# Kernel tuning notes

Measured on AMD Instinct MI355X. Metric: run time of the kernel, lower is better.

The kernel has to match this reference:

```python
import jax, jax.numpy as jnp
import numpy as np

L, H = 4, 8
BIAS_STEP = 25
LN_EPS = 1e-5

def make_pe(T, D):
    pos = np.arange(T)[:, None].astype(np.float32)
    div = np.exp(np.arange(0, D, 2).astype(np.float32) * (-np.log(10000.0) / D))
    pe = np.zeros((T, D), np.float32)
    pe[:, 0::2] = np.sin(pos * div)
    pe[:, 1::2] = np.cos(pos * div)
    return jnp.asarray(pe)

def make_band_mask(T):
    # (H, T, T) bool, True = masked out. Head h attends within |i-j| <= BIAS_STEP*(h+1).
    i = np.arange(T)
    dist = np.abs(i[:, None] - i[None, :])
    win = (np.arange(H) + 1) * BIAS_STEP
    return jnp.asarray(dist[None, :, :] > win[:, None, None])

def layer_norm(x, g, b):
    m = x.mean(-1, keepdims=True)
    v = ((x - m) ** 2).mean(-1, keepdims=True)
    return (x - m) * jax.lax.rsqrt(v + LN_EPS) * g + b

def setup_inputs() -> dict:
    key = jax.random.key(0)
    ks = jax.random.split(key, 16)
    s = 0.02
    BS, T, IN, D, FF, C = 8, 1000, 256, 512, 2048, 8
    return {
        'x': jax.random.normal(ks[0], (BS, T, IN), jnp.float32),
        'Wemb': jax.random.normal(ks[1], (D, IN), jnp.float32) * s,
        'bemb': jnp.zeros((D,), jnp.float32),
        'Wqkv': jax.random.normal(ks[2], (L, 3 * D, D), jnp.float32) * s,
        'bqkv': jnp.zeros((L, 3 * D), jnp.float32),
        'Wo': jax.random.normal(ks[3], (L, D, D), jnp.float32) * s,
        'bo': jnp.zeros((L, D), jnp.float32),
        'W1': jax.random.normal(ks[4], (L, FF, D), jnp.float32) * s,
        'b1f': jnp.zeros((L, FF), jnp.float32),
        'W2': jax.random.normal(ks[5], (L, D, FF), jnp.float32) * s,
        'b2f': jnp.zeros((L, D), jnp.float32),
        'g1': jnp.ones((L, D), jnp.float32),
        'be1': jnp.zeros((L, D), jnp.float32),
        'g2': jnp.ones((L, D), jnp.float32),
        'be2': jnp.zeros((L, D), jnp.float32),
        'Wcls': jax.random.normal(ks[6], (C, D), jnp.float32) * s,
        'bcls': jnp.zeros((C,), jnp.float32),
    }

def reference(x, Wemb, bemb, Wqkv, bqkv, Wo, bo, W1, b1f, W2, b2f, g1, be1, g2, be2, Wcls, bcls):
    bs, T, _ = x.shape
    D = Wemb.shape[0]
    dh = D // H
    h = x @ Wemb.T + bemb                     # (bs,T,D) input embedding
    h = h + make_pe(T, D)[None]               # sinusoidal PE (dropout=0)
    mask = make_band_mask(T)                  # (H,T,T)
    neg = jnp.finfo(h.dtype).min
    for l in range(L):                        # post-norm TransformerEncoderLayer
        qkv = h @ Wqkv[l].T + bqkv[l]
        q, k, v = jnp.split(qkv, 3, axis=-1)
        q = q.reshape(bs, T, H, dh).transpose(0, 2, 1, 3)
        k = k.reshape(bs, T, H, dh).transpose(0, 2, 1, 3)
        v = v.reshape(bs, T, H, dh).transpose(0, 2, 1, 3)
        s = jnp.einsum('bhqd,bhkd->bhqk', q, k) / jnp.sqrt(jnp.asarray(dh, h.dtype))
        s = jnp.where(mask[None], neg, s)
        a = jax.nn.softmax(s, axis=-1)
        o = jnp.einsum('bhqk,bhkd->bhqd', a, v).transpose(0, 2, 1, 3).reshape(bs, T, D)
        o = o @ Wo[l].T + bo[l]
        h = layer_norm(h + o, g1[l], be1[l])
        ff = jax.nn.relu(h @ W1[l].T + b1f[l]) @ W2[l].T + b2f[l]
        h = layer_norm(h + ff, g2[l], be2[l])
    pooled = h.max(axis=1)                    # global max pool over time (max_pool=True)
    logits = pooled @ Wcls.T + bcls
    return jax.nn.log_softmax(logits, axis=1)
```

## Files before the change

### kernel.cpp

```cpp
#include <hip/hip_runtime.h>
#include <math.h>

#define T_SEQ   1000
#define BATCH   8
#define DMODEL  512
#define NHEAD   8
#define DHEAD   64
#define FFDIM   2048
#define NLAYER  4
#define MROWS   (BATCH * T_SEQ)
#define TCHUNK  25
#define QKS     1024
#define VTS     1024

typedef __bf16 bf16x8 __attribute__((ext_vector_type(8)));
typedef __bf16 bf16x4 __attribute__((ext_vector_type(4)));
typedef float  f32x4  __attribute__((ext_vector_type(4)));
typedef float  f32x16 __attribute__((ext_vector_type(16)));

#define GL2LDS(g, l) \
    __builtin_amdgcn_global_load_lds((const __attribute__((address_space(1))) void*)(g), \
                                     (__attribute__((address_space(3))) void*)(l), 16, 0, 0)

struct F2BFArgs {
    const float* src[6];
    __bf16*      dst[6];
    int          off[7];
};

__global__ __launch_bounds__(256)
void f2bf_all(F2BFArgs a)
{
    const int blk = blockIdx.x;
    int seg = 0;
    #pragma unroll
    for (int s = 1; s < 6; ++s)
        if (blk >= a.off[s]) seg = s;
    const int i = (blk - a.off[seg]) * 1024 + threadIdx.x * 4;
    float4 v = *(const float4*)(a.src[seg] + i);
    bf16x4 o;
    o[0] = (__bf16)v.x; o[1] = (__bf16)v.y; o[2] = (__bf16)v.z; o[3] = (__bf16)v.w;
    *(bf16x4*)(a.dst[seg] + i) = o;
}

template<int MODE, bool RELU>
__global__ __launch_bounds__(256)
void gemm_bf16(const __bf16* __restrict__ A, const __bf16* __restrict__ B,
               const float* __restrict__ bias, __bf16* __restrict__ Cb,
               __bf16* __restrict__ Vt, int M, int N, int K)
{
    __shared__ __align__(16) __bf16 As[3][64 * 64];
    __shared__ __align__(16) __bf16 Bs[3][128 * 64];

    const int tid  = threadIdx.x;
    const int lane = tid & 63;
    const int w    = tid >> 6;
    const int wr   = w >> 1, wc = w & 1;

    const int gx  = gridDim.x;
    const int nwg = gx * gridDim.y;
    const int bid = blockIdx.y * gx + blockIdx.x;
    const int qc  = nwg >> 3, rc = nwg & 7;
    const int xcd = bid & 7, idx = bid >> 3;
    const int swz = (xcd < rc) ? xcd * (qc + 1) + idx
                               : rc * (qc + 1) + (xcd - rc) * qc + idx;
    const int row0 = (swz / gx) * 64;
    const int col0 = (swz % gx) * 128;

    size_t aoffg[2], boffg[4];
    int    ldso[4];
    #pragma unroll
    for (int p = 0; p < 4; ++p) {
        const int bo = p * 4096 + tid * 16;
        const int r  = bo >> 7;
        const int cs = (bo & 127) ^ ((r & 7) << 4);
        if (p < 2) aoffg[p] = (size_t)(row0 + r) * K * 2 + cs;
        boffg[p] = (size_t)(col0 + r) * K * 2 + cs;
        ldso[p]  = bo;
    }

    f32x4 acc[2][4];
    #pragma unroll
    for (int m = 0; m < 2; ++m)
        #pragma unroll
        for (int n = 0; n < 4; ++n) acc[m][n] = (f32x4)0.f;

    const char* gA = (const char*)A;
    const char* gB = (const char*)B;
    const int nt = K >> 6;

    auto STAGE = [&](int tt, int buf) {
        const size_t kb = (size_t)tt << 7;
        char* lA = (char*)As[buf];
        char* lB = (char*)Bs[buf];
        #pragma unroll
        for (int p = 0; p < 2; ++p) GL2LDS(gA + aoffg[p] + kb, lA + ldso[p]);
        #pragma unroll
        for (int p = 0; p < 4; ++p) GL2LDS(gB + boffg[p] + kb, lB + ldso[p]);
    };

    STAGE(0, 0);
    STAGE(1, 1);
    asm volatile("s_waitcnt vmcnt(6)" ::: "memory");
    __builtin_amdgcn_s_barrier();
    __builtin_amdgcn_sched_barrier(0);

    int bc = 0, bn = 2;
    for (int t = 0; t < nt; ++t) {
        if (t + 2 < nt) STAGE(t + 2, bn);
        const char* as = (const char*)As[bc];
        const char* bs = (const char*)Bs[bc];
        __builtin_amdgcn_s_setprio(1);
        #pragma unroll
        for (int ks = 0; ks < 2; ++ks) {
            bf16x8 af[2], bfr[4];
            const int cb = ks * 64 + (lane >> 4) * 16;
            #pragma unroll
            for (int m = 0; m < 2; ++m) {
                const int rr = wr * 32 + m * 16 + (lane & 15);
                af[m] = *(const bf16x8*)(as + rr * 128 + (cb ^ ((rr & 7) << 4)));
            }
            #pragma unroll
            for (int n = 0; n < 4; ++n) {
                const int rr = wc * 64 + n * 16 + (lane & 15);
                bfr[n] = *(const bf16x8*)(bs + rr * 128 + (cb ^ ((rr & 7) << 4)));
            }
            #pragma unroll
            for (int m = 0; m < 2; ++m)
                #pragma unroll
                for (int n = 0; n < 4; ++n)
                    acc[m][n] = __builtin_amdgcn_mfma_f32_16x16x32_bf16(af[m], bfr[n], acc[m][n], 0, 0, 0);
        }
        __builtin_amdgcn_s_setprio(0);
        if (t + 2 < nt) { asm volatile("s_waitcnt vmcnt(6)" ::: "memory"); }
        else            { asm volatile("s_waitcnt vmcnt(0)" ::: "memory"); }
        __builtin_amdgcn_s_barrier();
        __builtin_amdgcn_sched_barrier(0);
        bc = bc + 1; if (bc == 3) bc = 0;
        bn = bn + 1; if (bn == 3) bn = 0;
    }

    const int crow = (lane >> 4) * 4;
    const int ccol = lane & 15;

    if (MODE == 2 && col0 >= 1024) {
        __bf16* vtl = &Bs[0][0];
        #pragma unroll
        for (int n = 0; n < 4; ++n) {
            const int dl = wc * 64 + n * 16 + ccol;
            const float bv = bias[col0 + dl];
            #pragma unroll
            for (int m = 0; m < 2; ++m) {
                const int tl0 = wr * 32 + m * 16 + crow;
                #pragma unroll
                for (int r = 0; r < 4; ++r)
                    vtl[dl * 68 + tl0 + r] = (__bf16)(acc[m][n][r] + bv);
            }
        }
        __syncthreads();
        const int dbase = col0 - 1024;
        #pragma unroll
        for (int pass = 0; pass < 4; ++pass) {
            const int dl = pass * 32 + (tid >> 3);
            const int tc = (tid & 7) * 8;
            const int gr = row0 + tc;
            const bf16x8 vv = *(const bf16x8*)(vtl + dl * 68 + tc);
            const int bidx = gr / T_SEQ;
            const int tt   = gr - bidx * T_SEQ;
            __bf16* dst = Vt + (((size_t)(bidx * DMODEL + dbase + dl)) << 10) + tt;
            if (tt + 8 <= T_SEQ) {
                *(bf16x8*)dst = vv;
            } else {
                #pragma unroll
                for (int e = 0; e < 8; ++e) {
                    const int gre = gr + e;
                    const int be = gre / T_SEQ, te = gre - be * T_SEQ;
                    Vt[(((size_t)(be * DMODEL + dbase + dl)) << 10) + te] = vv[e];
                }
            }
        }
        return;
    }

    #pragma unroll
    for (int n = 0; n < 4; ++n) {
        const int gc = col0 + wc * 64 + n * 16 + ccol;
        const float bv = bias[gc];
        float freq = 0.f;
        if (MODE == 1) freq = __expf((float)(gc & ~1) * (-9.210340371976184f / (float)DMODEL));
        #pragma unroll
        for (int m = 0; m < 2; ++m) {
            const int gr0 = row0 + wr * 32 + m * 16 + crow;
            #pragma unroll
            for (int r = 0; r < 4; ++r) {
                const int gr = gr0 + r;
                float v = acc[m][n][r] + bv;
                if (MODE == 1) {
                    const int tt = gr % T_SEQ;
                    const float ang = (float)tt * freq;
                    v += (gc & 1) ? __cosf(ang) : __sinf(ang);
                }
                if (RELU) v = fmaxf(v, 0.f);
                if (MODE == 2) {
                    Cb[(size_t)gr * QKS + gc] = (__bf16)v;
                } else {
                    Cb[(size_t)gr * N + gc] = (__bf16)v;
                }
            }
        }
    }
}

__global__ __launch_bounds__(64)
void attn_mfma(const __bf16* __restrict__ qkb, const __bf16* __restrict__ vt,
               __bf16* __restrict__ o)
{
    const int wv   = blockIdx.x;
    const int lane = threadIdx.x;
    const int hh   = wv & 7;
    const int qt   = (wv >> 3) & 31;
    const int b    = wv >> 8;
    const int qb   = qt * 32;
    const int half = lane >> 5;
    const int ql   = lane & 31;
    const int i    = qb + ql;
    const int iq   = (i < T_SEQ) ? i : (T_SEQ - 1);
    const float C2 = 0.125f * 1.44269504089f;

    const __bf16* Q = qkb + (size_t)b * T_SEQ * QKS + hh * DHEAD;
    const __bf16* K = Q + 512;
    const __bf16* Vb = vt + (((size_t)b * DMODEL + hh * DHEAD) << 10);

    bf16x8 qf[4];
    {
        const __bf16* qrow = Q + (size_t)iq * QKS + half * 8;
        #pragma unroll
        for (int ds = 0; ds < 4; ++ds)
            qf[ds] = *(const bf16x8*)(qrow + ds * 16);
    }

    const int w = 25 * (hh + 1);
    const int kb_lo = (qb - w > 0 ? qb - w : 0) & ~31;
    const int kb_hi = (qb + 31 + w < T_SEQ - 1) ? (qb + 31 + w) : (T_SEQ - 1);
    const int spanv = (2 * w < T_SEQ - 1 - i + w) ? 2 * w : (T_SEQ - 1 - i + w);
    const unsigned span = (unsigned)spanv;

    float m2 = -1e9f, l = 0.f;
    f32x16 oa0 = (f32x16)0.f, oa1 = (f32x16)0.f;

    for (int kb = kb_lo; kb <= kb_hi; kb += 32) {
        f32x16 sv = (f32x16)0.f;
        {
            int krow = kb + ql; if (krow > T_SEQ - 1) krow = T_SEQ - 1;
            const __bf16* kr = K + (size_t)krow * QKS + half * 8;
            #pragma unroll
            for (int ds = 0; ds < 4; ++ds) {
                bf16x8 kf = *(const bf16x8*)(kr + ds * 16);
                sv = __builtin_amdgcn_mfma_f32_32x32x16_bf16(kf, qf[ds], sv, 0, 0, 0);
            }
        }

        const bool full = (kb >= qb + 31 - w) && (kb + 31 <= qb + w)
                       && (kb + 31 <= T_SEQ - 1);
        float s2[16];
        if (full) {
            #pragma unroll
            for (int r = 0; r < 16; ++r) s2[r] = sv[r] * C2;
        } else {
            const int base = kb - i + w;
            #pragma unroll
            for (int r = 0; r < 16; ++r) {
                const int kr = (r & 3) + 8 * (r >> 2) + 4 * half;
                const unsigned jrel = (unsigned)(base + kr);
                s2[r] = (jrel <= span) ? sv[r] * C2 : -1e9f;
            }
        }

        float mx = s2[0];
        #pragma unroll
        for (int r = 1; r < 16; ++r) mx = fmaxf(mx, s2[r]);
        mx = fmaxf(mx, __shfl_xor(mx, 32, 64));

        if (!__all(mx <= m2 + 8.0f)) {
            const float mnew  = fmaxf(m2, mx);
            const float scale = exp2f(m2 - mnew);
            m2 = mnew;
            l *= scale;
            oa0 *= scale;
            oa1 *= scale;
        }

        float p[16];
        float ps = 0.f;
        #pragma unroll
        for (int r = 0; r < 16; ++r) { p[r] = exp2f(s2[r] - m2); ps += p[r]; }
        ps += __shfl_xor(ps, 32, 64);
        l += ps;

        unsigned pk[8];
        #pragma unroll
        for (int t = 0; t < 8; ++t) {
            union { unsigned u; __bf16 h[2]; } cv;
            cv.h[0] = (__bf16)p[2 * t];
            cv.h[1] = (__bf16)p[2 * t + 1];
            pk[t] = cv.u;
        }
        unsigned y[8];
        #pragma unroll
        for (int t = 0; t < 8; ++t)
            y[t] = (unsigned)__shfl_xor((int)pk[t], 32, 64);

        union { unsigned u[4]; bf16x8 v; } pa0, pa1;
        if (half == 0) {
            pa0.u[0] = pk[0]; pa0.u[1] = pk[1]; pa0.u[2] = y[0];  pa0.u[3] = y[1];
            pa1.u[0] = pk[4]; pa1.u[1] = pk[5]; pa1.u[2] = y[4];  pa1.u[3] = y[5];
        } else {
            pa0.u[0] = y[2];  pa0.u[1] = y[3];  pa0.u[2] = pk[2]; pa0.u[3] = pk[3];
            pa1.u[0] = y[6];  pa1.u[1] = y[7];  pa1.u[2] = pk[6]; pa1.u[3] = pk[7];
        }

        #pragma unroll
        for (int ks = 0; ks < 2; ++ks) {
            const int kc = kb + ks * 16 + half * 8;
            #pragma unroll
            for (int dh = 0; dh < 2; ++dh) {
                const bf16x8 vf = *(const bf16x8*)(Vb + (((size_t)(dh * 32 + ql)) << 10) + kc);
                if (dh == 0)
                    oa0 = __builtin_amdgcn_mfma_f32_32x32x16_bf16(vf, ks ? pa1.v : pa0.v, oa0, 0, 0, 0);
                else
                    oa1 = __builtin_amdgcn_mfma_f32_32x32x16_bf16(vf, ks ? pa1.v : pa0.v, oa1, 0, 0, 0);
            }
        }
    }

    if (i < T_SEQ) {
        const float ri = 1.f / l;
        __bf16* orow = o + (size_t)(b * T_SEQ + i) * DMODEL + hh * DHEAD;
        #pragma unroll
        for (int g = 0; g < 4; ++g) {
            bf16x4 v0, v1;
            #pragma unroll
            for (int r = 0; r < 4; ++r) {
                v0[r] = (__bf16)(oa0[g * 4 + r] * ri);
                v1[r] = (__bf16)(oa1[g * 4 + r] * ri);
            }
            *(bf16x4*)(orow + g * 8 + half * 4)      = v0;
            *(bf16x4*)(orow + 32 + g * 8 + half * 4) = v1;
        }
    }
}

__global__ __launch_bounds__(256)
void add_ln(__bf16* __restrict__ hb, const __bf16* __restrict__ tbuf,
            const float* __restrict__ g, const float* __restrict__ b)
{
    const int row  = blockIdx.x * 4 + (threadIdx.x >> 6);
    const int lane = threadIdx.x & 63;
    __bf16*       hp = hb   + (size_t)row * DMODEL + lane * 8;
    const __bf16* tp = tbuf + (size_t)row * DMODEL + lane * 8;

    bf16x8 hv = *(const bf16x8*)hp;
    bf16x8 tv = *(const bf16x8*)tp;
    float xv[8];
    #pragma unroll
    for (int j = 0; j < 8; ++j) xv[j] = (float)hv[j] + (float)tv[j];

    float s = 0.f;
    #pragma unroll
    for (int j = 0; j < 8; ++j) s += xv[j];
    #pragma unroll
    for (int off = 32; off >= 1; off >>= 1) s += __shfl_xor(s, off, 64);
    float mean = s * (1.f / DMODEL);

    float vs = 0.f;
    #pragma unroll
    for (int j = 0; j < 8; ++j) { float d = xv[j] - mean; vs += d * d; }
    #pragma unroll
    for (int off = 32; off >= 1; off >>= 1) vs += __shfl_xor(vs, off, 64);
    float rstd = rsqrtf(vs * (1.f / DMODEL) + 1e-5f);

    float4 g0 = *(const float4*)(g + lane * 8);
    float4 g1 = *(const float4*)(g + lane * 8 + 4);
    float4 b0 = *(const float4*)(b + lane * 8);
    float4 b1 = *(const float4*)(b + lane * 8 + 4);
    float gg[8] = {g0.x, g0.y, g0.z, g0.w, g1.x, g1.y, g1.z, g1.w};
    float bb[8] = {b0.x, b0.y, b0.z, b0.w, b1.x, b1.y, b1.z, b1.w};

    bf16x8 ob;
    #pragma unroll
    for (int j = 0; j < 8; ++j)
        ob[j] = (__bf16)((xv[j] - mean) * rstd * gg[j] + bb[j]);
    *(bf16x8*)hp = ob;
}

__global__ __launch_bounds__(256)
void pool_p1(const __bf16* __restrict__ hb, float* __restrict__ part)
{
    const int bb  = blockIdx.x;
    const int tc  = blockIdx.y;
    const int tid = threadIdx.x;
    const int t0  = tc * (T_SEQ / TCHUNK);
    const __bf16* p = hb + ((size_t)bb * T_SEQ + t0) * DMODEL;

    float mx0 = -3.4e38f, mx1 = -3.4e38f;
    for (int t = 0; t < T_SEQ / TCHUNK; ++t) {
        mx0 = fmaxf(mx0, (float)p[(size_t)t * DMODEL + tid]);
        mx1 = fmaxf(mx1, (float)p[(size_t)t * DMODEL + 256 + tid]);
    }
    float* q = part + ((size_t)bb * TCHUNK + tc) * DMODEL;
    q[tid]       = mx0;
    q[tid + 256] = mx1;
}

__global__ __launch_bounds__(256)
void pool_p2(const float* __restrict__ part, const float* __restrict__ Wcls,
             const float* __restrict__ bcls, float* __restrict__ out)
{
    __shared__ float pooled[DMODEL];
    __shared__ float logits[8];
    const int bb  = blockIdx.x;
    const int tid = threadIdx.x;

    const float* q = part + (size_t)bb * TCHUNK * DMODEL;
    #pragma unroll
    for (int u = 0; u < 2; ++u) {
        const int d = tid + u * 256;
        float mx = -3.4e38f;
        for (int c = 0; c < TCHUNK; ++c) mx = fmaxf(mx, q[(size_t)c * DMODEL + d]);
        pooled[d] = mx;
    }
    __syncthreads();

    const int cls  = tid >> 5;
    const int lsub = tid & 31;
    const float* wr = Wcls + cls * DMODEL;
    float s = 0.f;
    #pragma unroll
    for (int u = 0; u < 16; ++u) {
        const int d = lsub + u * 32;
        s = fmaf(pooled[d], wr[d], s);
    }
    #pragma unroll
    for (int off = 16; off >= 1; off >>= 1) s += __shfl_xor(s, off, 32);
    if (lsub == 0) logits[cls] = s + bcls[cls];
    __syncthreads();

    if (tid == 0) {
        float mx = logits[0];
        for (int c = 1; c < 8; ++c) mx = fmaxf(mx, logits[c]);
        float se = 0.f;
        for (int c = 0; c < 8; ++c) se += expf(logits[c] - mx);
        float lse = logf(se) + mx;
        for (int c = 0; c < 8; ++c) out[bb * 8 + c] = logits[c] - lse;
    }
}

extern "C" void kernel_launch(void* const* d_in, const int* in_sizes, int n_in,
                              void* d_out, int out_size, void* d_ws, size_t ws_size,
                              hipStream_t stream)
{
    const float* x    = (const float*)d_in[0];
    const float* Wemb = (const float*)d_in[1];
    const float* bemb = (const float*)d_in[2];
    const float* Wqkv = (const float*)d_in[3];
    const float* bqkv = (const float*)d_in[4];
    const float* Wo   = (const float*)d_in[5];
    const float* bo   = (const float*)d_in[6];
    const float* W1   = (const float*)d_in[7];
    const float* b1f  = (const float*)d_in[8];
    const float* W2   = (const float*)d_in[9];
    const float* b2f  = (const float*)d_in[10];
    const float* g1   = (const float*)d_in[11];
    const float* be1  = (const float*)d_in[12];
    const float* g2   = (const float*)d_in[13];
    const float* be2  = (const float*)d_in[14];
    const float* Wcls = (const float*)d_in[15];
    const float* bcls = (const float*)d_in[16];
    float* out = (float*)d_out;

    __bf16* hb   = (__bf16*)d_ws;
    __bf16* qkb  = hb   + (size_t)MROWS * DMODEL;
    __bf16* vtb  = qkb  + (size_t)MROWS * QKS;
    __bf16* attb = vtb  + (size_t)BATCH * DMODEL * VTS;
    __bf16* ff1b = attb + (size_t)MROWS * DMODEL;
    __bf16* tmpB = ff1b + (size_t)MROWS * FFDIM;
    __bf16* xb   = tmpB + (size_t)MROWS * DMODEL;
    __bf16* wEmb = xb   + (size_t)MROWS * 256;
    __bf16* wQKV = wEmb + 512 * 256;
    __bf16* wWo  = wQKV + (size_t)NLAYER * 3 * DMODEL * DMODEL;
    __bf16* wW1  = wWo  + (size_t)NLAYER * DMODEL * DMODEL;
    __bf16* wW2  = wW1  + (size_t)NLAYER * FFDIM * DMODEL;
    float*  partF = (float*)(wW2 + (size_t)NLAYER * DMODEL * FFDIM);

    dim3 blk(256);

    {
        F2BFArgs a;
        const float* srcs[6] = {x, Wemb, Wqkv, Wo, W1, W2};
        __bf16*      dsts[6] = {xb, wEmb, wQKV, wWo, wW1, wW2};
        const int    nbs[6]  = {MROWS * 256 / 1024, 512 * 256 / 1024,
                                NLAYER * 3 * DMODEL * DMODEL / 1024,
                                NLAYER * DMODEL * DMODEL / 1024,
                                NLAYER * FFDIM * DMODEL / 1024,
                                NLAYER * DMODEL * FFDIM / 1024};
        a.off[0] = 0;
        for (int s = 0; s < 6; ++s) {
            a.src[s] = srcs[s];
            a.dst[s] = dsts[s];
            a.off[s + 1] = a.off[s] + nbs[s];
        }
        f2bf_all<<<dim3(a.off[6]), blk, 0, stream>>>(a);
    }

    gemm_bf16<1, false><<<dim3(4, 125), blk, 0, stream>>>(
        xb, wEmb, bemb, hb, nullptr, MROWS, DMODEL, 256);

    for (int l = 0; l < NLAYER; ++l) {
        gemm_bf16<2, false><<<dim3(12, 125), blk, 0, stream>>>(
            hb, wQKV + (size_t)l * 3 * DMODEL * DMODEL, bqkv + (size_t)l * 3 * DMODEL,
            qkb, vtb, MROWS, 3 * DMODEL, DMODEL);
        attn_mfma<<<dim3(2048), dim3(64), 0, stream>>>(qkb, vtb, attb);
        gemm_bf16<0, false><<<dim3(4, 125), blk, 0, stream>>>(
            attb, wWo + (size_t)l * DMODEL * DMODEL, bo + (size_t)l * DMODEL,
            tmpB, nullptr, MROWS, DMODEL, DMODEL);
        add_ln<<<dim3(MROWS / 4), blk, 0, stream>>>(
            hb, tmpB, g1 + (size_t)l * DMODEL, be1 + (size_t)l * DMODEL);
        gemm_bf16<0, true><<<dim3(16, 125), blk, 0, stream>>>(
            hb, wW1 + (size_t)l * FFDIM * DMODEL, b1f + (size_t)l * FFDIM,
            ff1b, nullptr, MROWS, FFDIM, DMODEL);
        gemm_bf16<0, false><<<dim3(4, 125), blk, 0, stream>>>(
            ff1b, wW2 + (size_t)l * DMODEL * FFDIM, b2f + (size_t)l * DMODEL,
            tmpB, nullptr, MROWS, DMODEL, FFDIM);
        add_ln<<<dim3(MROWS / 4), blk, 0, stream>>>(
            hb, tmpB, g2 + (size_t)l * DMODEL, be2 + (size_t)l * DMODEL);
    }

    pool_p1<<<dim3(BATCH, TCHUNK), blk, 0, stream>>>(hb, partF);
    pool_p2<<<dim3(BATCH), blk, 0, stream>>>(partF, Wcls, bcls, out);
}
```

Before: 600.0 us.

## Split-K the FFN down-projection into two halves and sum in layer norm

The W2 GEMM (K=2048) now runs as a two-way split-K launch over a third grid dimension. Each half writes a separate bf16 partial, the second reusing the attention buffer, and a new add_ln3 kernel sums both partials with the residual before normalizing. This doubles the workgroup count for a GEMM that otherwise launches only 500 tiles, improving CU occupancy and shortening the long serial K loop. In exchange it adds an extra bf16 write and read of a full activation tensor and rounds each partial sum to bf16. The attention key loop also gets an unroll-2 pragma.

```diff
diff --git a/kernel.cpp b/kernel.cpp
--- a/kernel.cpp
+++ b/kernel.cpp
@@ -47,7 +47,7 @@
 __global__ __launch_bounds__(256)
 void gemm_bf16(const __bf16* __restrict__ A, const __bf16* __restrict__ B,
                const float* __restrict__ bias, __bf16* __restrict__ Cb,
-               __bf16* __restrict__ Vt, int M, int N, int K)
+               __bf16* __restrict__ C2, int M, int N, int K, int lda, int ldb)
 {
     __shared__ __align__(16) __bf16 As[3][64 * 64];
     __shared__ __align__(16) __bf16 Bs[3][128 * 64];
@@ -57,15 +57,25 @@
     const int w    = tid >> 6;
     const int wr   = w >> 1, wc = w & 1;
 
-    const int gx  = gridDim.x;
-    const int nwg = gx * gridDim.y;
-    const int bid = blockIdx.y * gx + blockIdx.x;
+    const int gx  = gridDim.x, gy = gridDim.y, gz = gridDim.z;
+    const int nwg = gx * gy * gz;
+    const int bid = (blockIdx.z * gy + blockIdx.y) * gx + blockIdx.x;
     const int qc  = nwg >> 3, rc = nwg & 7;
     const int xcd = bid & 7, idx = bid >> 3;
     const int swz = (xcd < rc) ? xcd * (qc + 1) + idx
                                : rc * (qc + 1) + (xcd - rc) * qc + idx;
-    const int row0 = (swz / gx) * 64;
-    const int col0 = (swz % gx) * 128;
+    const int bx   = swz % gx;
+    const int rest = swz / gx;
+    const int by   = rest % gy;
+    const int bz   = rest / gy;
+    const int row0 = by * 64;
+    const int col0 = bx * 128;
+
+    const __bf16* Ae = A;
+    const __bf16* Be = B;
+    const float*  be = bias;
+    __bf16*       Co = Cb;
+    if (MODE == 3 && bz) { Ae += K; Be += K; be = nullptr; Co = C2; }
 
     size_t aoffg[2], boffg[4];
     int    ldso[4];
@@ -74,8 +84,8 @@
         const int bo = p * 4096 + tid * 16;
         const int r  = bo >> 7;
         const int cs = (bo & 127) ^ ((r & 7) << 4);
-        if (p < 2) aoffg[p] = (size_t)(row0 + r) * K * 2 + cs;
-        boffg[p] = (size_t)(col0 + r) * K * 2 + cs;
+        if (p < 2) aoffg[p] = (size_t)(row0 + r) * lda * 2 + cs;
+        boffg[p] = (size_t)(col0 + r) * ldb * 2 + cs;
         ldso[p]  = bo;
     }
 
@@ -85,8 +95,8 @@
         #pragma unroll
         for (int n = 0; n < 4; ++n) acc[m][n] = (f32x4)0.f;
 
-    const char* gA = (const char*)A;
-    const char* gB = (const char*)B;
+    const char* gA = (const char*)Ae;
+    const char* gB = (const char*)Be;
     const int nt = K >> 6;
 
     auto STAGE = [&](int tt, int buf) {
@@ -148,7 +158,7 @@
         #pragma unroll
         for (int n = 0; n < 4; ++n) {
             const int dl = wc * 64 + n * 16 + ccol;
-            const float bv = bias[col0 + dl];
+            const float bv = be[col0 + dl];
             #pragma unroll
             for (int m = 0; m < 2; ++m) {
                 const int tl0 = wr * 32 + m * 16 + crow;
@@ -167,15 +177,15 @@
             const bf16x8 vv = *(const bf16x8*)(vtl + dl * 68 + tc);
             const int bidx = gr / T_SEQ;
             const int tt   = gr - bidx * T_SEQ;
-            __bf16* dst = Vt + (((size_t)(bidx * DMODEL + dbase + dl)) << 10) + tt;
+            __bf16* dst = C2 + (((size_t)(bidx * DMODEL + dbase + dl)) << 10) + tt;
             if (tt + 8 <= T_SEQ) {
                 *(bf16x8*)dst = vv;
             } else {
                 #pragma unroll
                 for (int e = 0; e < 8; ++e) {
                     const int gre = gr + e;
-                    const int be = gre / T_SEQ, te = gre - be * T_SEQ;
-                    Vt[(((size_t)(be * DMODEL + dbase + dl)) << 10) + te] = vv[e];
+                    const int bbe = gre / T_SEQ, te = gre - bbe * T_SEQ;
+                    C2[(((size_t)(bbe * DMODEL + dbase + dl)) << 10) + te] = vv[e];
                 }
             }
         }
@@ -185,7 +195,7 @@
     #pragma unroll
     for (int n = 0; n < 4; ++n) {
         const int gc = col0 + wc * 64 + n * 16 + ccol;
-        const float bv = bias[gc];
+        const float bv = be ? be[gc] : 0.f;
         float freq = 0.f;
         if (MODE == 1) freq = __expf((float)(gc & ~1) * (-9.210340371976184f / (float)DMODEL));
         #pragma unroll
@@ -202,9 +212,9 @@
                 }
                 if (RELU) v = fmaxf(v, 0.f);
                 if (MODE == 2) {
-                    Cb[(size_t)gr * QKS + gc] = (__bf16)v;
+                    Co[(size_t)gr * QKS + gc] = (__bf16)v;
                 } else {
-                    Cb[(size_t)gr * N + gc] = (__bf16)v;
+                    Co[(size_t)gr * N + gc] = (__bf16)v;
                 }
             }
         }
@@ -248,6 +258,7 @@
     float m2 = -1e9f, l = 0.f;
     f32x16 oa0 = (f32x16)0.f, oa1 = (f32x16)0.f;
 
+    #pragma unroll 2
     for (int kb = kb_lo; kb <= kb_hi; kb += 32) {
         f32x16 sv = (f32x16)0.f;
         {
@@ -364,6 +375,53 @@
     float xv[8];
     #pragma unroll
     for (int j = 0; j < 8; ++j) xv[j] = (float)hv[j] + (float)tv[j];
+
+    float s = 0.f;
+    #pragma unroll
+    for (int j = 0; j < 8; ++j) s += xv[j];
+    #pragma unroll
+    for (int off = 32; off >= 1; off >>= 1) s += __shfl_xor(s, off, 64);
+    float mean = s * (1.f / DMODEL);
+
+    float vs = 0.f;
+    #pragma unroll
+    for (int j = 0; j < 8; ++j) { float d = xv[j] - mean; vs += d * d; }
+    #pragma unroll
+    for (int off = 32; off >= 1; off >>= 1) vs += __shfl_xor(vs, off, 64);
+    float rstd = rsqrtf(vs * (1.f / DMODEL) + 1e-5f);
+
+    float4 g0 = *(const float4*)(g + lane * 8);
+    float4 g1 = *(const float4*)(g + lane * 8 + 4);
+    float4 b0 = *(const float4*)(b + lane * 8);
+    float4 b1 = *(const float4*)(b + lane * 8 + 4);
+    float gg[8] = {g0.x, g0.y, g0.z, g0.w, g1.x, g1.y, g1.z, g1.w};
+    float bb[8] = {b0.x, b0.y, b0.z, b0.w, b1.x, b1.y, b1.z, b1.w};
+
+    bf16x8 ob;
+    #pragma unroll
+    for (int j = 0; j < 8; ++j)
+        ob[j] = (__bf16)((xv[j] - mean) * rstd * gg[j] + bb[j]);
+    *(bf16x8*)hp = ob;
+}
+
+__global__ __launch_bounds__(256)
+void add_ln3(__bf16* __restrict__ hb, const __bf16* __restrict__ ta,
+             const __bf16* __restrict__ tb2, const float* __restrict__ g,
+             const float* __restrict__ b)
+{
+    const int row  = blockIdx.x * 4 + (threadIdx.x >> 6);
+    const int lane = threadIdx.x & 63;
+    __bf16*       hp = hb  + (size_t)row * DMODEL + lane * 8;
+    const __bf16* pa = ta  + (size_t)row * DMODEL + lane * 8;
+    const __bf16* pb = tb2 + (size_t)row * DMODEL + lane * 8;
+
+    bf16x8 hv = *(const bf16x8*)hp;
+    bf16x8 av = *(const bf16x8*)pa;
+    bf16x8 bv2 = *(const bf16x8*)pb;
+    float xv[8];
+    #pragma unroll
+    for (int j = 0; j < 8; ++j)
+        xv[j] = (float)hv[j] + (float)av[j] + (float)bv2[j];
 
     float s = 0.f;
     #pragma unroll
@@ -513,26 +571,26 @@
     }
 
     gemm_bf16<1, false><<<dim3(4, 125), blk, 0, stream>>>(
-        xb, wEmb, bemb, hb, nullptr, MROWS, DMODEL, 256);
+        xb, wEmb, bemb, hb, nullptr, MROWS, DMODEL, 256, 256, 256);
 
     for (int l = 0; l < NLAYER; ++l) {
         gemm_bf16<2, false><<<dim3(12, 125), blk, 0, stream>>>(
             hb, wQKV + (size_t)l * 3 * DMODEL * DMODEL, bqkv + (size_t)l * 3 * DMODEL,
-            qkb, vtb, MROWS, 3 * DMODEL, DMODEL);
+            qkb, vtb, MROWS, 3 * DMODEL, DMODEL, DMODEL, DMODEL);
         attn_mfma<<<dim3(2048), dim3(64), 0, stream>>>(qkb, vtb, attb);
         gemm_bf16<0, false><<<dim3(4, 125), blk, 0, stream>>>(
             attb, wWo + (size_t)l * DMODEL * DMODEL, bo + (size_t)l * DMODEL,
-            tmpB, nullptr, MROWS, DMODEL, DMODEL);
+            tmpB, nullptr, MROWS, DMODEL, DMODEL, DMODEL, DMODEL);
         add_ln<<<dim3(MROWS / 4), blk, 0, stream>>>(
             hb, tmpB, g1 + (size_t)l * DMODEL, be1 + (size_t)l * DMODEL);
         gemm_bf16<0, true><<<dim3(16, 125), blk, 0, stream>>>(
             hb, wW1 + (size_t)l * FFDIM * DMODEL, b1f + (size_t)l * FFDIM,
-            ff1b, nullptr, MROWS, FFDIM, DMODEL);
-        gemm_bf16<0, false><<<dim3(4, 125), blk, 0, stream>>>(
+            ff1b, nullptr, MROWS, FFDIM, DMODEL, DMODEL, DMODEL);
+        gemm_bf16<3, false><<<dim3(4, 125, 2), blk, 0, stream>>>(
             ff1b, wW2 + (size_t)l * DMODEL * FFDIM, b2f + (size_t)l * DMODEL,
-            tmpB, nullptr, MROWS, DMODEL, FFDIM);
-        add_ln<<<dim3(MROWS / 4), blk, 0, stream>>>(
-            hb, tmpB, g2 + (size_t)l * DMODEL, be2 + (size_t)l * DMODEL);
+            tmpB, attb, MROWS, DMODEL, FFDIM / 2, FFDIM, FFDIM);
+        add_ln3<<<dim3(MROWS / 4), blk, 0, stream>>>(
+            hb, tmpB, attb, g2 + (size_t)l * DMODEL, be2 + (size_t)l * DMODEL);
     }
 
     pool_p1<<<dim3(BATCH, TCHUNK), blk, 0, stream>>>(hb, partF);
```

Result: slower. 621.3 us (+3.6%).

## Split attention key range in two partial blocks and merge with combine kernel

Applied to the files above, without the earlier changes.

Attention work for each (batch, query tile, head) is split across two 64-thread blocks, each handling half of the banded key blocks. Each writes an unnormalized partial output plus running max and sum, and a new combine kernel rescales and merges them. The aim is to double the number of wavefronts, since 2048 single-wave blocks underfill the GPU, and to shorten the critical path for wide-window heads. The cost is an extra launch, a round trip of partial outputs through global memory reusing ff1b/tmpB, and bf16 rounding of unnormalized partials.

```diff
diff --git a/kernel.cpp b/kernel.cpp
--- a/kernel.cpp
+++ b/kernel.cpp
@@ -212,14 +212,15 @@
 }
 
 __global__ __launch_bounds__(64)
-void attn_mfma(const __bf16* __restrict__ qkb, const __bf16* __restrict__ vt,
-               __bf16* __restrict__ o)
-{
-    const int wv   = blockIdx.x;
+void attn_part(const __bf16* __restrict__ qkb, const __bf16* __restrict__ vt,
+               __bf16* __restrict__ opart, float* __restrict__ ml)
+{
+    const int j    = blockIdx.x;
+    const int hf   = j & 1;
+    const int hh   = (j >> 1) & 7;
+    const int qt   = (j >> 4) & 31;
+    const int b    = j >> 9;
     const int lane = threadIdx.x;
-    const int hh   = wv & 7;
-    const int qt   = (wv >> 3) & 31;
-    const int b    = wv >> 8;
     const int qb   = qt * 32;
     const int half = lane >> 5;
     const int ql   = lane & 31;
@@ -245,10 +246,15 @@
     const int spanv = (2 * w < T_SEQ - 1 - i + w) ? 2 * w : (T_SEQ - 1 - i + w);
     const unsigned span = (unsigned)spanv;
 
+    const int nkb = ((kb_hi - kb_lo) >> 5) + 1;
+    const int c0  = (nkb + 1) >> 1;
+    const int kst = hf ? (kb_lo + c0 * 32) : kb_lo;
+    const int ken = hf ? kb_hi : (kb_lo + c0 * 32 - 32);
+
     float m2 = -1e9f, l = 0.f;
     f32x16 oa0 = (f32x16)0.f, oa1 = (f32x16)0.f;
 
-    for (int kb = kb_lo; kb <= kb_hi; kb += 32) {
+    for (int kb = kst; kb <= ken; kb += 32) {
         f32x16 sv = (f32x16)0.f;
         {
             int krow = kb + ql; if (krow > T_SEQ - 1) krow = T_SEQ - 1;
@@ -333,20 +339,60 @@
         }
     }
 
-    if (i < T_SEQ) {
-        const float ri = 1.f / l;
-        __bf16* orow = o + (size_t)(b * T_SEQ + i) * DMODEL + hh * DHEAD;
-        #pragma unroll
-        for (int g = 0; g < 4; ++g) {
-            bf16x4 v0, v1;
-            #pragma unroll
-            for (int r = 0; r < 4; ++r) {
-                v0[r] = (__bf16)(oa0[g * 4 + r] * ri);
-                v1[r] = (__bf16)(oa1[g * 4 + r] * ri);
-            }
-            *(bf16x4*)(orow + g * 8 + half * 4)      = v0;
-            *(bf16x4*)(orow + 32 + g * 8 + half * 4) = v1;
-        }
+    __bf16* orow = opart + (size_t)j * 2048 + ql * 64;
+    #pragma unroll
+    for (int g = 0; g < 4; ++g) {
+        bf16x4 v0, v1;
+        #pragma unroll
+        for (int r = 0; r < 4; ++r) {
+            v0[r] = (__bf16)oa0[g * 4 + r];
+            v1[r] = (__bf16)oa1[g * 4 + r];
+        }
+        *(bf16x4*)(orow + g * 8 + half * 4)      = v0;
+        *(bf16x4*)(orow + 32 + g * 8 + half * 4) = v1;
+    }
+    if (lane < 32) {
+        ml[(size_t)j * 64 + ql * 2]     = m2;
+        ml[(size_t)j * 64 + ql * 2 + 1] = l;
+    }
+}
+
+__global__ __launch_bounds__(64)
+void attn_comb(const __bf16* __restrict__ opart, const float* __restrict__ ml,
+               __bf16* __restrict__ o)
+{
+    const int j    = blockIdx.x;
+    const int hh   = j & 7;
+    const int qt   = (j >> 3) & 31;
+    const int b    = j >> 8;
+    const int lane = threadIdx.x;
+    const int ql   = lane & 31;
+    const int dh   = lane >> 5;
+    const int i    = qt * 32 + ql;
+    if (i >= T_SEQ) return;
+
+    const int pj0 = j * 2, pj1 = pj0 + 1;
+    const float m0 = ml[(size_t)pj0 * 64 + ql * 2];
+    const float l0 = ml[(size_t)pj0 * 64 + ql * 2 + 1];
+    const float m1 = ml[(size_t)pj1 * 64 + ql * 2];
+    const float l1 = ml[(size_t)pj1 * 64 + ql * 2 + 1];
+    const float mN = fmaxf(m0, m1);
+    const float e0 = exp2f(m0 - mN);
+    const float e1 = exp2f(m1 - mN);
+    const float ri = 1.f / (l0 * e0 + l1 * e1);
+
+    const __bf16* p0 = opart + (size_t)pj0 * 2048 + ql * 64 + dh * 32;
+    const __bf16* p1 = opart + (size_t)pj1 * 2048 + ql * 64 + dh * 32;
+    __bf16* orow = o + (size_t)(b * T_SEQ + i) * DMODEL + hh * DHEAD + dh * 32;
+    #pragma unroll
+    for (int g = 0; g < 4; ++g) {
+        const bf16x8 a = *(const bf16x8*)(p0 + g * 8);
+        const bf16x8 c = *(const bf16x8*)(p1 + g * 8);
+        bf16x8 r;
+        #pragma unroll
+        for (int e = 0; e < 8; ++e)
+            r[e] = (__bf16)(((float)a[e] * e0 + (float)c[e] * e1) * ri);
+        *(bf16x8*)(orow + g * 8) = r;
     }
 }
 
@@ -492,6 +538,9 @@
     __bf16* wW2  = wW1  + (size_t)NLAYER * FFDIM * DMODEL;
     float*  partF = (float*)(wW2 + (size_t)NLAYER * DMODEL * FFDIM);
 
+    __bf16* opart = ff1b;
+    float*  mlbuf = (float*)tmpB;
+
     dim3 blk(256);
 
     {
@@ -519,7 +568,8 @@
         gemm_bf16<2, false><<<dim3(12, 125), blk, 0, stream>>>(
             hb, wQKV + (size_t)l * 3 * DMODEL * DMODEL, bqkv + (size_t)l * 3 * DMODEL,
             qkb, vtb, MROWS, 3 * DMODEL, DMODEL);
-        attn_mfma<<<dim3(2048), dim3(64), 0, stream>>>(qkb, vtb, attb);
+        attn_part<<<dim3(4096), dim3(64), 0, stream>>>(qkb, vtb, opart, mlbuf);
+        attn_comb<<<dim3(2048), dim3(64), 0, stream>>>(opart, mlbuf, attb);
         gemm_bf16<0, false><<<dim3(4, 125), blk, 0, stream>>>(
             attb, wWo + (size_t)l * DMODEL * DMODEL, bo + (size_t)l * DMODEL,
             tmpB, nullptr, MROWS, DMODEL, DMODEL);
```

Result: slower. 654.0 us (+9.0%).
